# Performance work log

Measured on AMD Instinct MI355X. Metric: run time of the kernel, lower is better.

## Reference

```python
import jax, jax.numpy as jnp
import numpy as np

LAMBD = 0.05

def _mlp(y, W0, b0, W1, b1, W2, b2, W3, b3):
    h = jax.nn.relu(y @ W0.T + b0)
    h = jax.nn.relu(h @ W1.T + b1)
    h = jax.nn.relu(h @ W2.T + b2)
    return h @ W3.T + b3  # [N, 1]


def setup_inputs() -> dict:
    key = jax.random.key(0)
    ks = jax.random.split(key, 8)
    B, N, D = 4096, 20000, 784
    s = lambda fan_in: 1.0 / np.sqrt(fan_in)
    return {
        "x": jax.random.normal(ks[0], (B, D), jnp.float32),
        "y": jax.random.normal(ks[1], (N, D), jnp.float32),
        "nu": jax.random.uniform(ks[2], (N,), jnp.float32, 0.1, 1.0),
        "W0": jax.random.normal(ks[3], (512, D), jnp.float32) * s(D),
        "b0": jnp.zeros((512,), jnp.float32),
        "W1": jax.random.normal(ks[4], (256, 512), jnp.float32) * s(512),
        "b1": jnp.zeros((256,), jnp.float32),
        "W2": jax.random.normal(ks[5], (128, 256), jnp.float32) * s(256),
        "b2": jnp.zeros((128,), jnp.float32),
        "W3": jax.random.normal(ks[6], (1, 128), jnp.float32) * s(128),
        "b3": jnp.zeros((1,), jnp.float32),
    }


def reference(x, y, nu, W0, b0, W1, b1, W2, b2, W3, b3):
    # squared-distance cost matrix [B, N], normalized by mean(|y|^2)
    sy2 = jnp.sum(y * y, axis=1)            # [N]
    normalization = sy2.mean()
    cxy = (jnp.sum(x * x, axis=1, keepdims=True) + sy2[None, :]
           - 2.0 * (x @ y.T)) / normalization  # [B, N]
    psiy = _mlp(y, W0, b0, W1, b1, W2, b2, W3, b3)[:, 0]  # [N]
    # entropic semi-dual: -lambd * logsumexp((psi(y) - c(x,y))/lambd + log nu)
    z = (psiy[None, :] - cxy) / LAMBD + jnp.log(nu)[None, :]
    out = -LAMBD * jax.nn.logsumexp(z, axis=1) + psiy.mean()  # [B]
    return out
```

## Files before the change

### kernel.cpp

```cpp
#include <hip/hip_runtime.h>
#include <math.h>
#include <stdint.h>
#include <stddef.h>

#define B_ROWS 4096
#define N_REAL 20000
#define NP2    20224
#define NJT2   79
#define NRT    32
#define D_IN   784
#define DP2    800
#define NKS    25
#define NKT    13
#define YBLK   316
#define XBLK   64
#define LAMBD  0.05f
#define LN2    0.69314718055994530942f
#define QS     (4.5f / 127.f)
#define QINV   (127.f / 4.5f)

typedef __attribute__((ext_vector_type(8))) short bf16x8;
typedef __attribute__((ext_vector_type(4))) float f32x4;
typedef __attribute__((ext_vector_type(4))) int   i32x4;

typedef const unsigned int __attribute__((address_space(1)))* gas_u32p;
typedef unsigned int __attribute__((address_space(3)))* las_u32p;

static __device__ __forceinline__ void gload_lds16(const void* g, void* l) {
  __builtin_amdgcn_global_load_lds((gas_u32p)g, (las_u32p)l, 16, 0, 0);
}

static __device__ __forceinline__ float bf2f(short s) {
  union { unsigned u; float f; } c;
  c.u = ((unsigned)(unsigned short)s) << 16;
  return c.f;
}
static __device__ __forceinline__ short f2bf(float f) {
  union { float f; unsigned u; } c;
  c.f = f;
  unsigned r = (c.u + 0x7fffu + ((c.u >> 16) & 1u)) >> 16;
  return (short)(unsigned short)r;
}
static __device__ __forceinline__ unsigned q4c(float a, float b, float c, float d) {
  int x0 = min(127, max(-127, (int)rintf(a * QINV))) & 255;
  int x1 = min(127, max(-127, (int)rintf(b * QINV))) & 255;
  int x2 = min(127, max(-127, (int)rintf(c * QINV))) & 255;
  int x3 = min(127, max(-127, (int)rintf(d * QINV))) & 255;
  return (unsigned)(x0 | (x1 << 8) | (x2 << 16) | (x3 << 24));
}

__global__ void k_prep(const float* __restrict__ ysrc, const float* __restrict__ xsrc,
                       unsigned char* __restrict__ y_i8, unsigned char* __restrict__ x_i8,
                       short* __restrict__ y_bf, float* __restrict__ sy2,
                       float* __restrict__ x2,
                       const float* __restrict__ W0, const float* __restrict__ W1,
                       const float* __restrict__ W2, short* __restrict__ W0b,
                       short* __restrict__ W1b, short* __restrict__ W2b,
                       unsigned* __restrict__ ctr) {
  const int b = blockIdx.x, t = threadIdx.x;
  if (b == 0 && t == 0) *ctr = 0u;

  if (b >= YBLK + XBLK) {
    const int wb_ = b - (YBLK + XBLK);
    const float* src; short* dst; int r, cs, cp;
    if (wb_ < 512)      { r = wb_;       src = W0; dst = W0b; cs = D_IN; cp = DP2; }
    else if (wb_ < 768) { r = wb_ - 512; src = W1; dst = W1b; cs = 512;  cp = 512; }
    else                { r = wb_ - 768; src = W2; dst = W2b; cs = 256;  cp = 256; }
    const float* sp = src + (size_t)r * cs;
    short* dp = dst + (size_t)r * cp;
    for (int c = t; c < cp; c += 256)
      dp[c] = f2bf(c < cs ? sp[c] : 0.f);
    return;
  }

  const float* src; unsigned char* di8; float* rowsum;
  int rows_real, trshift, g; bool wbf;
  if (b < YBLK) { src = ysrc; di8 = y_i8; rowsum = sy2;
                  rows_real = N_REAL; trshift = 8; g = b; wbf = true; }
  else          { src = xsrc; di8 = x_i8; rowsum = x2;
                  rows_real = B_ROWS; trshift = 7; g = b - YBLK; wbf = false; }
  const int q = t & 3, r = t >> 2;
  const int grow = g * 64 + r;
  const int tile1 = grow >> trshift, sub1 = grow & ((1 << trshift) - 1);
  const size_t imgBytes = (size_t)64 << trshift;
  const float* sp = src + (size_t)grow * D_IN;
  const bool realRow = grow < rows_real;
  float sq = 0.f;

  for (int kt = 0; kt < NKT; ++kt) {
    const int c0 = kt * 64 + q * 16;
    float v[16];
    if (realRow && c0 < D_IN) {
      #pragma unroll
      for (int u = 0; u < 4; ++u) {
        float4 w4 = *(const float4*)(sp + c0 + u * 4);
        v[u*4+0] = w4.x; v[u*4+1] = w4.y; v[u*4+2] = w4.z; v[u*4+3] = w4.w;
        sq += w4.x * w4.x + w4.y * w4.y + w4.z * w4.z + w4.w * w4.w;
      }
    } else {
      #pragma unroll
      for (int e = 0; e < 16; ++e) v[e] = 0.f;
    }
    uint4 pk;
    pk.x = q4c(v[0],  v[1],  v[2],  v[3]);
    pk.y = q4c(v[4],  v[5],  v[6],  v[7]);
    pk.z = q4c(v[8],  v[9],  v[10], v[11]);
    pk.w = q4c(v[12], v[13], v[14], v[15]);
    *(uint4*)(di8 + (size_t)(tile1 * NKT + kt) * imgBytes
              + ((size_t)((q << trshift) + sub1) << 4)) = pk;
    if (wbf) {
      const int ks = kt * 2 + (q >> 1);
      if (ks < NKS) {
        const int tile2 = grow >> 8, sub2 = grow & 255;
        const int oct = (q & 1) * 2;
        short* dp = y_bf + (size_t)(tile2 * NKS + ks) * 8192
                  + ((size_t)(oct * 256 + sub2) << 3);
        bf16x8 o0, o1;
        #pragma unroll
        for (int e = 0; e < 8; ++e) { o0[e] = f2bf(v[e]); o1[e] = f2bf(v[8 + e]); }
        *(bf16x8*)dp = o0;
        *(bf16x8*)(dp + 2048) = o1;
      }
    }
  }

  sq += __shfl_xor(sq, 1, 4);
  sq += __shfl_xor(sq, 2, 4);
  if (q == 0 && realRow) rowsum[grow] = sq;
}

template <bool TA>
__global__ __launch_bounds__(256) void k_gemmf(const short* __restrict__ A,
                                               const short* __restrict__ Bm,
                                               const float* __restrict__ bias,
                                               short* __restrict__ C,
                                               int K, int Ncols,
                                               const float* __restrict__ W3c,
                                               const float* __restrict__ b3c,
                                               float* __restrict__ psiOut,
                                               const float* __restrict__ sy2n,
                                               float* __restrict__ scaln) {
  extern __shared__ short L[];
  __shared__ float pbuf[256];
  const int t = threadIdx.x;
  const int rb = blockIdx.y, cb = blockIdx.x;

  if (sy2n != nullptr && rb == NP2 / 128) {
    if (cb != 0) return;
    __shared__ float red[4];
    float a = 0.f;
    for (int j = t; j < N_REAL; j += 256) a += sy2n[j];
    #pragma unroll
    for (int m = 1; m < 64; m <<= 1) a += __shfl_xor(a, m, 64);
    if ((t & 63) == 0) red[t >> 6] = a;
    __syncthreads();
    if (t == 0) {
      float norm = (red[0] + red[1] + red[2] + red[3]) / (float)N_REAL;
      scaln[0] = norm;
      scaln[1] = 1.0f / norm;
      scaln[2] = 2.0f / (norm * LAMBD * LN2);
    }
    return;
  }

  const int lane = t & 63, wave = t >> 6;
  const int lr = lane & 15, lg = lane >> 4;
  const int wrow = (wave >> 1) * 64, wcol = (wave & 1) * 64;
  const int KS = K >> 5;
  const int wb = wave * 512;

  const int prow = t & 127, psel = t >> 7;
  const short* aS0; const short* aS1; int aStep;
  if constexpr (TA) {
    const short* base = A + (size_t)((rb >> 1) * NKS) * 8192
                      + ((size_t)((rb & 1) * 128 + prow) << 3);
    aS0 = base + (size_t)(psel * 2048);
    aS1 = base + (size_t)((2 + psel) * 2048);
    aStep = 8192;
  } else {
    const short* base = A + (size_t)(rb * 128 + prow) * K;
    aS0 = base + psel * 8;
    aS1 = base + (2 + psel) * 8;
    aStep = 32;
  }
  const short* bBase = Bm + (size_t)(cb * 128 + prow) * K;
  const short* bS0 = bBase + psel * 8;
  const short* bS1 = bBase + (2 + psel) * 8;

  auto stage = [&](int s) {
    short* Lb = L + (s % 3) * 8192;
    gload_lds16(aS0 + (size_t)s * aStep, Lb + wb);
    gload_lds16(aS1 + (size_t)s * aStep, Lb + 2048 + wb);
    gload_lds16(bS0 + (size_t)s * 32,    Lb + 4096 + wb);
    gload_lds16(bS1 + (size_t)s * 32,    Lb + 4096 + 2048 + wb);
  };

  f32x4 acc[4][4];
  #pragma unroll
  for (int mi = 0; mi < 4; ++mi)
    #pragma unroll
    for (int ni = 0; ni < 4; ++ni)
      acc[mi][ni] = (f32x4){0.f, 0.f, 0.f, 0.f};

  stage(0);
  stage(1);
  asm volatile("s_waitcnt vmcnt(4)" ::: "memory");
  __builtin_amdgcn_s_barrier();
  __builtin_amdgcn_sched_barrier(0);

  const int aro = (wrow + lr) * 8;
  const int bro = (wcol + lr) * 8;
  for (int ks = 0; ks < KS; ++ks) {
    if (ks + 2 < KS) stage(ks + 2);
    const short* LA = L + (ks % 3) * 8192 + lg * 1024;
    const short* LB = LA + 4096;
    bf16x8 b0 = *(const bf16x8*)&LB[bro];
    bf16x8 b1 = *(const bf16x8*)&LB[bro + 128];
    bf16x8 b2 = *(const bf16x8*)&LB[bro + 256];
    bf16x8 b3 = *(const bf16x8*)&LB[bro + 384];
    bf16x8 a0 = *(const bf16x8*)&LA[aro];
    bf16x8 a1 = *(const bf16x8*)&LA[aro + 128];
    bf16x8 a2v = *(const bf16x8*)&LA[aro + 256];
    bf16x8 a3v = *(const bf16x8*)&LA[aro + 384];
    __builtin_amdgcn_s_setprio(1);
    #pragma unroll
    for (int ni = 0; ni < 4; ++ni) {
      bf16x8 bv = ni == 0 ? b0 : ni == 1 ? b1 : ni == 2 ? b2 : b3;
      acc[0][ni] = __builtin_amdgcn_mfma_f32_16x16x32_bf16(a0, bv, acc[0][ni], 0, 0, 0);
      acc[1][ni] = __builtin_amdgcn_mfma_f32_16x16x32_bf16(a1, bv, acc[1][ni], 0, 0, 0);
      acc[2][ni] = __builtin_amdgcn_mfma_f32_16x16x32_bf16(a2v, bv, acc[2][ni], 0, 0, 0);
      acc[3][ni] = __builtin_amdgcn_mfma_f32_16x16x32_bf16(a3v, bv, acc[3][ni], 0, 0, 0);
    }
    __builtin_amdgcn_s_setprio(0);
    if (ks + 2 < KS) {
      asm volatile("s_waitcnt vmcnt(4)" ::: "memory");
      __builtin_amdgcn_s_barrier();
      __builtin_amdgcn_sched_barrier(0);
    } else if (ks + 1 < KS) {
      asm volatile("s_waitcnt vmcnt(0)" ::: "memory");
      __builtin_amdgcn_s_barrier();
      __builtin_amdgcn_sched_barrier(0);
    }
  }

  if (psiOut == nullptr) {
    #pragma unroll
    for (int ni = 0; ni < 4; ++ni) {
      const int col = cb * 128 + wcol + ni * 16 + lr;
      const float bv = bias[col];
      #pragma unroll
      for (int mi = 0; mi < 4; ++mi) {
        const int row0 = rb * 128 + wrow + mi * 16 + lg * 4;
        #pragma unroll
        for (int r = 0; r < 4; ++r)
          C[(size_t)(row0 + r) * Ncols + col] = f2bf(fmaxf(acc[mi][ni][r] + bv, 0.f));
      }
    }
  } else {
    float part[4][4];
    #pragma unroll
    for (int mi = 0; mi < 4; ++mi)
      #pragma unroll
      for (int r = 0; r < 4; ++r) part[mi][r] = 0.f;
    #pragma unroll
    for (int ni = 0; ni < 4; ++ni) {
      const int col = wcol + ni * 16 + lr;
      const float bv = bias[col];
      const float w3 = W3c[col];
      #pragma unroll
      for (int mi = 0; mi < 4; ++mi)
        #pragma unroll
        for (int r = 0; r < 4; ++r)
          part[mi][r] += fmaxf(acc[mi][ni][r] + bv, 0.f) * w3;
    }
    #pragma unroll
    for (int mi = 0; mi < 4; ++mi)
      #pragma unroll
      for (int r = 0; r < 4; ++r) {
        float s = part[mi][r];
        s += __shfl_xor(s, 1, 16);
        s += __shfl_xor(s, 2, 16);
        s += __shfl_xor(s, 4, 16);
        s += __shfl_xor(s, 8, 16);
        part[mi][r] = s;
      }
    if (lr == 0) {
      #pragma unroll
      for (int mi = 0; mi < 4; ++mi)
        #pragma unroll
        for (int r = 0; r < 4; ++r)
          pbuf[(wave & 1) * 128 + (wave >> 1) * 64 + mi * 16 + lg * 4 + r] = part[mi][r];
    }
    __syncthreads();
    if (t < 128) psiOut[rb * 128 + t] = pbuf[t] + pbuf[t + 128] + b3c[0];
  }
}

__global__ void k_a2(const float* __restrict__ psi, const float* __restrict__ sy2,
                     const float* __restrict__ nu, const float* __restrict__ scal,
                     float* __restrict__ a2raw, float* __restrict__ maxp,
                     float* __restrict__ sump, unsigned* __restrict__ ctr,
                     float* __restrict__ scalw) {
  const int j = blockIdx.x * 256 + threadIdx.x;
  const float invn = scal[1];
  float a = -1e30f, p = 0.f;
  if (j < NP2) {
    if (j < N_REAL) {
      p = psi[j];
      a = (p - sy2[j] * invn) * (1.0f / (LAMBD * LN2)) + log2f(nu[j]);
    }
    a2raw[j] = a;
  }
  __shared__ float redm[4], reds[4];
  __shared__ int lastFlag;
  #pragma unroll
  for (int m = 1; m < 64; m <<= 1) {
    a = fmaxf(a, __shfl_xor(a, m, 64));
    p += __shfl_xor(p, m, 64);
  }
  const int t = threadIdx.x;
  if ((t & 63) == 0) { redm[t >> 6] = a; reds[t >> 6] = p; }
  __syncthreads();
  if (t == 0) {
    maxp[blockIdx.x] = fmaxf(fmaxf(redm[0], redm[1]), fmaxf(redm[2], redm[3]));
    sump[blockIdx.x] = reds[0] + reds[1] + reds[2] + reds[3];
    __threadfence();
    lastFlag = (atomicAdd(ctr, 1u) == (unsigned)(gridDim.x - 1));
  }
  __syncthreads();
  if (lastFlag) {
    __threadfence();
    float am = -1e30f, s = 0.f;
    for (int i = t; i < (int)gridDim.x; i += 256) {
      am = fmaxf(am, maxp[i]);
      s += sump[i];
    }
    #pragma unroll
    for (int m = 1; m < 64; m <<= 1) {
      am = fmaxf(am, __shfl_xor(am, m, 64));
      s += __shfl_xor(s, m, 64);
    }
    if ((t & 63) == 0) { redm[t >> 6] = am; reds[t >> 6] = s; }
    __syncthreads();
    if (t == 0) {
      scalw[3] = fmaxf(fmaxf(redm[0], redm[1]), fmaxf(redm[2], redm[3]));
      scalw[4] = (reds[0] + reds[1] + reds[2] + reds[3]) / (float)N_REAL;
    }
  }
}

__global__ __launch_bounds__(512, 4) void k_flash(const unsigned char* __restrict__ x_t,
                                                  const unsigned char* __restrict__ y_t,
                                                  const float* __restrict__ a2raw,
                                                  const float* __restrict__ scal,
                                                  float* __restrict__ parts) {
  extern __shared__ char Lsh[];
  const int t = threadIdx.x;
  const int lane = t & 63, wave = t >> 6;
  const int lr = lane & 15, lg = lane >> 4;
  const int wr = wave >> 2, wc = wave & 3;
  const int rbt = blockIdx.x, jt = blockIdx.y;

  const float s2c1 = QS * QS * scal[2];
  const float A2 = scal[3];

  const int t16 = t * 16;
  const int wb = wave * 1024;
  const int aoff = (lg * 128 + wr * 64 + lr) * 16;
  const int boff = (lg * 256 + wc * 64 + lr) * 16;

  const unsigned char* As = x_t + (size_t)(rbt * NKT) * 8192 + t16;
  const unsigned char* Bs = y_t + (size_t)(jt * NKT) * 16384 + t16;

  i32x4 acc[4][4];
  #pragma unroll
  for (int mi = 0; mi < 4; ++mi)
    #pragma unroll
    for (int ni = 0; ni < 4; ++ni)
      acc[mi][ni] = (i32x4){0, 0, 0, 0};

  auto stage = [&](int s) {
    char* Lb = Lsh + (s % 3) * 24576;
    const unsigned char* An = As + (size_t)s * 8192;
    const unsigned char* Bn = Bs + (size_t)s * 16384;
    gload_lds16(An,        Lb + wb);
    gload_lds16(Bn,        Lb + 8192 + wb);
    gload_lds16(Bn + 8192, Lb + 16384 + wb);
  };

  stage(0);
  stage(1);
  asm volatile("s_waitcnt vmcnt(3)" ::: "memory");
  __builtin_amdgcn_s_barrier();
  __builtin_amdgcn_sched_barrier(0);

  #pragma unroll
  for (int ks = 0; ks < NKT; ++ks) {
    if (ks + 2 < NKT) stage(ks + 2);
    const char* LA = Lsh + (ks % 3) * 24576;
    const char* LB = LA + 8192;
    i32x4 b0 = *(const i32x4*)(LB + boff);
    i32x4 b1 = *(const i32x4*)(LB + boff + 256);
    i32x4 b2 = *(const i32x4*)(LB + boff + 512);
    i32x4 b3 = *(const i32x4*)(LB + boff + 768);
    i32x4 a0 = *(const i32x4*)(LA + aoff);
    i32x4 a1 = *(const i32x4*)(LA + aoff + 256);
    i32x4 a2v = *(const i32x4*)(LA + aoff + 512);
    i32x4 a3v = *(const i32x4*)(LA + aoff + 768);
    __builtin_amdgcn_s_setprio(1);
    #pragma unroll
    for (int ni = 0; ni < 4; ++ni) {
      i32x4 bv = ni == 0 ? b0 : ni == 1 ? b1 : ni == 2 ? b2 : b3;
      acc[0][ni] = __builtin_amdgcn_mfma_i32_16x16x64_i8(a0, bv, acc[0][ni], 0, 0, 0);
      acc[1][ni] = __builtin_amdgcn_mfma_i32_16x16x64_i8(a1, bv, acc[1][ni], 0, 0, 0);
      acc[2][ni] = __builtin_amdgcn_mfma_i32_16x16x64_i8(a2v, bv, acc[2][ni], 0, 0, 0);
      acc[3][ni] = __builtin_amdgcn_mfma_i32_16x16x64_i8(a3v, bv, acc[3][ni], 0, 0, 0);
    }
    __builtin_amdgcn_s_setprio(0);
    if (ks + 2 < NKT) {
      asm volatile("s_waitcnt vmcnt(3)" ::: "memory");
      __builtin_amdgcn_s_barrier();
      __builtin_amdgcn_sched_barrier(0);
    } else if (ks + 1 < NKT) {
      asm volatile("s_waitcnt vmcnt(0)" ::: "memory");
      __builtin_amdgcn_s_barrier();
      __builtin_amdgcn_sched_barrier(0);
    }
  }

  const int colb = jt * 256 + wc * 64 + lr;
  float av[4];
  #pragma unroll
  for (int ni = 0; ni < 4; ++ni)
    av[ni] = a2raw[colb + ni * 16] - A2;
  #pragma unroll
  for (int mi = 0; mi < 4; ++mi)
    #pragma unroll
    for (int r = 0; r < 4; ++r) {
      const int row = rbt * 128 + wr * 64 + mi * 16 + lg * 4 + r;
      float s = exp2f((float)acc[mi][0][r] * s2c1 + av[0])
              + exp2f((float)acc[mi][1][r] * s2c1 + av[1])
              + exp2f((float)acc[mi][2][r] * s2c1 + av[2])
              + exp2f((float)acc[mi][3][r] * s2c1 + av[3]);
      s += __shfl_xor(s, 1, 16);
      s += __shfl_xor(s, 2, 16);
      s += __shfl_xor(s, 4, 16);
      s += __shfl_xor(s, 8, 16);
      if (lr == 0)
        parts[(size_t)row * (NJT2 * 4) + jt * 4 + wc] = s;
    }
}

__global__ void k_comb(const float* __restrict__ parts, const float* __restrict__ x2,
                       const float* __restrict__ scal, float* __restrict__ out) {
  const int wave = threadIdx.x >> 6, lane = threadIdx.x & 63;
  const int row = blockIdx.x * 4 + wave;
  const float* pr = parts + (size_t)row * (NJT2 * 4);
  float s = 0.f;
  for (int i = lane; i < NJT2 * 4; i += 64) s += pr[i];
  #pragma unroll
  for (int m = 1; m < 64; m <<= 1) s += __shfl_xor(s, m, 64);
  if (lane == 0)
    out[row] = -(LAMBD * LN2) * (scal[3] + log2f(s)) + x2[row] * scal[1] + scal[4];
}

extern "C" void kernel_launch(void* const* d_in, const int* in_sizes, int n_in,
                              void* d_out, int out_size, void* d_ws, size_t ws_size,
                              hipStream_t stream) {
  const float* x  = (const float*)d_in[0];
  const float* y  = (const float*)d_in[1];
  const float* nu = (const float*)d_in[2];
  const float* W0 = (const float*)d_in[3];
  const float* b0 = (const float*)d_in[4];
  const float* W1 = (const float*)d_in[5];
  const float* b1 = (const float*)d_in[6];
  const float* W2 = (const float*)d_in[7];
  const float* b2 = (const float*)d_in[8];
  const float* W3 = (const float*)d_in[9];
  const float* b3 = (const float*)d_in[10];
  float* out = (float*)d_out;

  char* w = (char*)d_ws;
  auto alloc = [&](size_t bytes) {
    char* p = w;
    w += (bytes + 255) & ~(size_t)255;
    return p;
  };
  unsigned char* y_i8 = (unsigned char*)alloc((size_t)NJT2 * NKT * 16384);
  unsigned char* x_i8 = (unsigned char*)alloc((size_t)NRT * NKT * 8192);
  short* y_bf  = (short*)alloc((size_t)(NP2 / 256) * NKS * 8192 * 2);
  short* W0b   = (short*)alloc((size_t)512 * DP2 * 2);
  short* W1b   = (short*)alloc((size_t)256 * 512 * 2);
  short* W2b   = (short*)alloc((size_t)128 * 256 * 2);
  short* H1    = (short*)alloc((size_t)NP2 * 512 * 2);
  short* H2    = (short*)alloc((size_t)NP2 * 256 * 2);
  float* sy2   = (float*)alloc((size_t)N_REAL * 4);
  float* x2    = (float*)alloc((size_t)B_ROWS * 4);
  float* psi   = (float*)alloc((size_t)NP2 * 4);
  float* a2raw = (float*)alloc((size_t)NP2 * 4);
  float* maxp  = (float*)alloc(128 * 4);
  float* sump  = (float*)alloc(128 * 4);
  float* scal  = (float*)alloc(64 * 4);
  unsigned* ctr = (unsigned*)alloc(256);
  float* parts = (float*)alloc((size_t)B_ROWS * NJT2 * 4 * 4);

  k_prep<<<dim3(YBLK + XBLK + 896), dim3(256), 0, stream>>>(y, x, y_i8, x_i8, y_bf,
                                                            sy2, x2, W0, W1, W2,
                                                            W0b, W1b, W2b, ctr);

  hipFuncSetAttribute((const void*)k_gemmf<true>, hipFuncAttributeMaxDynamicSharedMemorySize, 49152);
  hipFuncSetAttribute((const void*)k_gemmf<false>, hipFuncAttributeMaxDynamicSharedMemorySize, 49152);
  k_gemmf<true><<<dim3(4, NP2 / 128 + 1), dim3(256), 49152, stream>>>(
      y_bf, W0b, b0, H1, DP2, 512, nullptr, nullptr, nullptr, sy2, scal);
  k_gemmf<false><<<dim3(2, NP2 / 128), dim3(256), 49152, stream>>>(
      H1, W1b, b1, H2, 512, 256, nullptr, nullptr, nullptr, nullptr, nullptr);
  k_gemmf<false><<<dim3(1, NP2 / 128), dim3(256), 49152, stream>>>(
      H2, W2b, b2, nullptr, 256, 128, W3, b3, psi, nullptr, nullptr);

  k_a2<<<dim3(NP2 / 256), dim3(256), 0, stream>>>(psi, sy2, nu, scal, a2raw,
                                                  maxp, sump, ctr, scal);

  hipFuncSetAttribute((const void*)k_flash, hipFuncAttributeMaxDynamicSharedMemorySize, 73728);
  k_flash<<<dim3(NRT, NJT2), dim3(512), 73728, stream>>>(x_i8, y_i8, a2raw, scal, parts);
  k_comb<<<dim3(B_ROWS / 4), dim3(256), 0, stream>>>(parts, x2, scal, out);
}
```

Measured before the change: 193.8 us.

## Enlarge flash int8 GEMM tile to 256x256 with matching x layout

Doubles the row tile of the int8 cost-matrix kernel from 128 to 256 rows. Each wave now covers 64x128 outputs, holding an 8-wide accumulator array instead of 4-wide. The x int8 layout is made to match the y layout, and the partial-sum buffer shrinks from 4 to 2 partials per column tile. The aim is to roughly halve global/LDS traffic per MFMA and cut the combine work. The cost is higher register pressure (launch bound lowered from 4 to 2), more LDS per block, and half as many blocks (16x79 grid) to fill the GPU.

```diff
diff --git a/kernel.cpp b/kernel.cpp
--- a/kernel.cpp
+++ b/kernel.cpp
@@ -7,13 +7,14 @@
 #define N_REAL 20000
 #define NP2    20224
 #define NJT2   79
-#define NRT    32
+#define NRT    16
 #define D_IN   784
 #define DP2    800
 #define NKS    25
 #define NKT    13
 #define YBLK   316
 #define XBLK   64
+#define PW     158
 #define LAMBD  0.05f
 #define LN2    0.69314718055994530942f
 #define QS     (4.5f / 127.f)
@@ -74,15 +75,14 @@
   }
 
   const float* src; unsigned char* di8; float* rowsum;
-  int rows_real, trshift, g; bool wbf;
+  int rows_real, g; bool wbf;
   if (b < YBLK) { src = ysrc; di8 = y_i8; rowsum = sy2;
-                  rows_real = N_REAL; trshift = 8; g = b; wbf = true; }
+                  rows_real = N_REAL; g = b; wbf = true; }
   else          { src = xsrc; di8 = x_i8; rowsum = x2;
-                  rows_real = B_ROWS; trshift = 7; g = b - YBLK; wbf = false; }
+                  rows_real = B_ROWS; g = b - YBLK; wbf = false; }
   const int q = t & 3, r = t >> 2;
   const int grow = g * 64 + r;
-  const int tile1 = grow >> trshift, sub1 = grow & ((1 << trshift) - 1);
-  const size_t imgBytes = (size_t)64 << trshift;
+  const int tile1 = grow >> 8, sub1 = grow & 255;
   const float* sp = src + (size_t)grow * D_IN;
   const bool realRow = grow < rows_real;
   float sq = 0.f;
@@ -106,15 +106,14 @@
     pk.y = q4c(v[4],  v[5],  v[6],  v[7]);
     pk.z = q4c(v[8],  v[9],  v[10], v[11]);
     pk.w = q4c(v[12], v[13], v[14], v[15]);
-    *(uint4*)(di8 + (size_t)(tile1 * NKT + kt) * imgBytes
-              + ((size_t)((q << trshift) + sub1) << 4)) = pk;
+    *(uint4*)(di8 + (size_t)(tile1 * NKT + kt) * 16384
+              + ((size_t)(q * 256 + sub1) << 4)) = pk;
     if (wbf) {
       const int ks = kt * 2 + (q >> 1);
       if (ks < NKS) {
-        const int tile2 = grow >> 8, sub2 = grow & 255;
         const int oct = (q & 1) * 2;
-        short* dp = y_bf + (size_t)(tile2 * NKS + ks) * 8192
-                  + ((size_t)(oct * 256 + sub2) << 3);
+        short* dp = y_bf + (size_t)(tile1 * NKS + ks) * 8192
+                  + ((size_t)(oct * 256 + sub1) << 3);
         bf16x8 o0, o1;
         #pragma unroll
         for (int e = 0; e < 8; ++e) { o0[e] = f2bf(v[e]); o1[e] = f2bf(v[8 + e]); }
@@ -349,7 +348,7 @@
   }
 }
 
-__global__ __launch_bounds__(512, 4) void k_flash(const unsigned char* __restrict__ x_t,
+__global__ __launch_bounds__(512, 2) void k_flash(const unsigned char* __restrict__ x_t,
                                                   const unsigned char* __restrict__ y_t,
                                                   const float* __restrict__ a2raw,
                                                   const float* __restrict__ scal,
@@ -358,7 +357,7 @@
   const int t = threadIdx.x;
   const int lane = t & 63, wave = t >> 6;
   const int lr = lane & 15, lg = lane >> 4;
-  const int wr = wave >> 2, wc = wave & 3;
+  const int wr = wave >> 1, wc = wave & 1;
   const int rbt = blockIdx.x, jt = blockIdx.y;
 
   const float s2c1 = QS * QS * scal[2];
@@ -366,59 +365,59 @@
 
   const int t16 = t * 16;
   const int wb = wave * 1024;
-  const int aoff = (lg * 128 + wr * 64 + lr) * 16;
-  const int boff = (lg * 256 + wc * 64 + lr) * 16;
-
-  const unsigned char* As = x_t + (size_t)(rbt * NKT) * 8192 + t16;
+  const int aoff = (lg * 256 + wr * 64 + lr) * 16;
+  const int boff = (lg * 256 + wc * 128 + lr) * 16;
+
+  const unsigned char* As = x_t + (size_t)(rbt * NKT) * 16384 + t16;
   const unsigned char* Bs = y_t + (size_t)(jt * NKT) * 16384 + t16;
 
-  i32x4 acc[4][4];
+  i32x4 acc[4][8];
   #pragma unroll
   for (int mi = 0; mi < 4; ++mi)
     #pragma unroll
-    for (int ni = 0; ni < 4; ++ni)
+    for (int ni = 0; ni < 8; ++ni)
       acc[mi][ni] = (i32x4){0, 0, 0, 0};
 
   auto stage = [&](int s) {
-    char* Lb = Lsh + (s % 3) * 24576;
-    const unsigned char* An = As + (size_t)s * 8192;
+    char* Lb = Lsh + (s % 3) * 32768;
+    const unsigned char* An = As + (size_t)s * 16384;
     const unsigned char* Bn = Bs + (size_t)s * 16384;
-    gload_lds16(An,        Lb + wb);
-    gload_lds16(Bn,        Lb + 8192 + wb);
-    gload_lds16(Bn + 8192, Lb + 16384 + wb);
+    gload_lds16(An,         Lb + wb);
+    gload_lds16(An + 8192,  Lb + 8192 + wb);
+    gload_lds16(Bn,         Lb + 16384 + wb);
+    gload_lds16(Bn + 8192,  Lb + 24576 + wb);
   };
 
   stage(0);
   stage(1);
-  asm volatile("s_waitcnt vmcnt(3)" ::: "memory");
+  asm volatile("s_waitcnt vmcnt(4)" ::: "memory");
   __builtin_amdgcn_s_barrier();
   __builtin_amdgcn_sched_barrier(0);
 
   #pragma unroll
   for (int ks = 0; ks < NKT; ++ks) {
     if (ks + 2 < NKT) stage(ks + 2);
-    const char* LA = Lsh + (ks % 3) * 24576;
-    const char* LB = LA + 8192;
-    i32x4 b0 = *(const i32x4*)(LB + boff);
-    i32x4 b1 = *(const i32x4*)(LB + boff + 256);
-    i32x4 b2 = *(const i32x4*)(LB + boff + 512);
-    i32x4 b3 = *(const i32x4*)(LB + boff + 768);
-    i32x4 a0 = *(const i32x4*)(LA + aoff);
-    i32x4 a1 = *(const i32x4*)(LA + aoff + 256);
-    i32x4 a2v = *(const i32x4*)(LA + aoff + 512);
-    i32x4 a3v = *(const i32x4*)(LA + aoff + 768);
+    const char* LA = Lsh + (ks % 3) * 32768;
+    const char* LB = LA + 16384;
+    i32x4 bf[8];
+    #pragma unroll
+    for (int ni = 0; ni < 8; ++ni)
+      bf[ni] = *(const i32x4*)(LB + boff + ni * 256);
+    i32x4 af[4];
+    #pragma unroll
+    for (int mi = 0; mi < 4; ++mi)
+      af[mi] = *(const i32x4*)(LA + aoff + mi * 256);
     __builtin_amdgcn_s_setprio(1);
     #pragma unroll
-    for (int ni = 0; ni < 4; ++ni) {
-      i32x4 bv = ni == 0 ? b0 : ni == 1 ? b1 : ni == 2 ? b2 : b3;
-      acc[0][ni] = __builtin_amdgcn_mfma_i32_16x16x64_i8(a0, bv, acc[0][ni], 0, 0, 0);
-      acc[1][ni] = __builtin_amdgcn_mfma_i32_16x16x64_i8(a1, bv, acc[1][ni], 0, 0, 0);
-      acc[2][ni] = __builtin_amdgcn_mfma_i32_16x16x64_i8(a2v, bv, acc[2][ni], 0, 0, 0);
-      acc[3][ni] = __builtin_amdgcn_mfma_i32_16x16x64_i8(a3v, bv, acc[3][ni], 0, 0, 0);
+    for (int ni = 0; ni < 8; ++ni) {
+      acc[0][ni] = __builtin_amdgcn_mfma_i32_16x16x64_i8(af[0], bf[ni], acc[0][ni], 0, 0, 0);
+      acc[1][ni] = __builtin_amdgcn_mfma_i32_16x16x64_i8(af[1], bf[ni], acc[1][ni], 0, 0, 0);
+      acc[2][ni] = __builtin_amdgcn_mfma_i32_16x16x64_i8(af[2], bf[ni], acc[2][ni], 0, 0, 0);
+      acc[3][ni] = __builtin_amdgcn_mfma_i32_16x16x64_i8(af[3], bf[ni], acc[3][ni], 0, 0, 0);
     }
     __builtin_amdgcn_s_setprio(0);
     if (ks + 2 < NKT) {
-      asm volatile("s_waitcnt vmcnt(3)" ::: "memory");
+      asm volatile("s_waitcnt vmcnt(4)" ::: "memory");
       __builtin_amdgcn_s_barrier();
       __builtin_amdgcn_sched_barrier(0);
     } else if (ks + 1 < NKT) {
@@ -428,26 +427,26 @@
     }
   }
 
-  const int colb = jt * 256 + wc * 64 + lr;
-  float av[4];
-  #pragma unroll
-  for (int ni = 0; ni < 4; ++ni)
+  const int colb = jt * 256 + wc * 128 + lr;
+  float av[8];
+  #pragma unroll
+  for (int ni = 0; ni < 8; ++ni)
     av[ni] = a2raw[colb + ni * 16] - A2;
   #pragma unroll
   for (int mi = 0; mi < 4; ++mi)
     #pragma unroll
     for (int r = 0; r < 4; ++r) {
-      const int row = rbt * 128 + wr * 64 + mi * 16 + lg * 4 + r;
-      float s = exp2f((float)acc[mi][0][r] * s2c1 + av[0])
-              + exp2f((float)acc[mi][1][r] * s2c1 + av[1])
-              + exp2f((float)acc[mi][2][r] * s2c1 + av[2])
-              + exp2f((float)acc[mi][3][r] * s2c1 + av[3]);
+      const int row = rbt * 256 + wr * 64 + mi * 16 + lg * 4 + r;
+      float s = 0.f;
+      #pragma unroll
+      for (int ni = 0; ni < 8; ++ni)
+        s += exp2f((float)acc[mi][ni][r] * s2c1 + av[ni]);
       s += __shfl_xor(s, 1, 16);
       s += __shfl_xor(s, 2, 16);
       s += __shfl_xor(s, 4, 16);
       s += __shfl_xor(s, 8, 16);
       if (lr == 0)
-        parts[(size_t)row * (NJT2 * 4) + jt * 4 + wc] = s;
+        parts[(size_t)row * PW + jt * 2 + wc] = s;
     }
 }
 
@@ -455,9 +454,9 @@
                        const float* __restrict__ scal, float* __restrict__ out) {
   const int wave = threadIdx.x >> 6, lane = threadIdx.x & 63;
   const int row = blockIdx.x * 4 + wave;
-  const float* pr = parts + (size_t)row * (NJT2 * 4);
+  const float* pr = parts + (size_t)row * PW;
   float s = 0.f;
-  for (int i = lane; i < NJT2 * 4; i += 64) s += pr[i];
+  for (int i = lane; i < PW; i += 64) s += pr[i];
   #pragma unroll
   for (int m = 1; m < 64; m <<= 1) s += __shfl_xor(s, m, 64);
   if (lane == 0)
@@ -487,7 +486,7 @@
     return p;
   };
   unsigned char* y_i8 = (unsigned char*)alloc((size_t)NJT2 * NKT * 16384);
-  unsigned char* x_i8 = (unsigned char*)alloc((size_t)NRT * NKT * 8192);
+  unsigned char* x_i8 = (unsigned char*)alloc((size_t)NRT * NKT * 16384);
   short* y_bf  = (short*)alloc((size_t)(NP2 / 256) * NKS * 8192 * 2);
   short* W0b   = (short*)alloc((size_t)512 * DP2 * 2);
   short* W1b   = (short*)alloc((size_t)256 * 512 * 2);
@@ -502,7 +501,7 @@
   float* sump  = (float*)alloc(128 * 4);
   float* scal  = (float*)alloc(64 * 4);
   unsigned* ctr = (unsigned*)alloc(256);
-  float* parts = (float*)alloc((size_t)B_ROWS * NJT2 * 4 * 4);
+  float* parts = (float*)alloc((size_t)B_ROWS * PW * 4);
 
   k_prep<<<dim3(YBLK + XBLK + 896), dim3(256), 0, stream>>>(y, x, y_i8, x_i8, y_bf,
                                                             sy2, x2, W0, W1, W2,
@@ -520,7 +519,7 @@
   k_a2<<<dim3(NP2 / 256), dim3(256), 0, stream>>>(psi, sy2, nu, scal, a2raw,
                                                   maxp, sump, ctr, scal);
 
-  hipFuncSetAttribute((const void*)k_flash, hipFuncAttributeMaxDynamicSharedMemorySize, 73728);
-  k_flash<<<dim3(NRT, NJT2), dim3(512), 73728, stream>>>(x_i8, y_i8, a2raw, scal, parts);
+  hipFuncSetAttribute((const void*)k_flash, hipFuncAttributeMaxDynamicSharedMemorySize, 98304);
+  k_flash<<<dim3(NRT, NJT2), dim3(512), 98304, stream>>>(x_i8, y_i8, a2raw, scal, parts);
   k_comb<<<dim3(B_ROWS / 4), dim3(256), 0, stream>>>(parts, x2, scal, out);
 }
```

Measured after the change: 186.5 us. 3.7% less time.
